# Performance work log

Measured on AMD Instinct MI355X. Metric: run time of the kernel, lower is better.

## Reference

```python
import jax, jax.numpy as jnp
import numpy as np

NUM_STAB = 0.001  # numerical_stabilizer from relu_kernel_transformation


def relu_kernel(data, proj):
    """ReLU random-feature kernel: data [B,L,H,D], proj [M,D] -> [B,L,H,M]."""
    ratio = 1.0 / jnp.sqrt(jnp.asarray(proj.shape[0], jnp.float32))
    data_dash = ratio * jnp.einsum('blhd,md->blhm', data, proj)
    return jax.nn.relu(data_dash) + NUM_STAB


def setup_inputs() -> dict:
    key = jax.random.key(0)
    k1, k2, k3, k4 = jax.random.split(key, 4)
    B, L, H, D, M = 2, 4096, 8, 64, 256
    return {
        'query': jax.random.normal(k1, (B, L, H, D), jnp.float32),
        'key_t': jax.random.normal(k2, (B, L, H, D), jnp.float32),
        'value': jax.random.normal(k3, (B, L, H, D), jnp.float32),
        'projection_matrix': jax.random.normal(k4, (M, D), jnp.float32),
    }


def reference(query, key_t, value, projection_matrix):
    # Kernel feature maps [B,L,H,M]
    qp = relu_kernel(query, projection_matrix)
    kp = relu_kernel(key_t, projection_matrix)
    # Causal path operates in [L,B,H,*] layout
    qs = jnp.transpose(qp, (1, 0, 2, 3))     # [L,B,H,M]
    ks = jnp.transpose(kp, (1, 0, 2, 3))     # [L,B,H,M]
    vs = jnp.transpose(value, (1, 0, 2, 3))  # [L,B,H,D]

    B, H, M = qs.shape[1], qs.shape[2], qs.shape[3]
    D = vs.shape[3]
    init = (jnp.zeros((B, H, M, D), qs.dtype),  # running sum of k outer v
            jnp.zeros((B, H, M), qs.dtype))     # running sum of k

    def step(carry, inp):
        kv_sum, k_sum = carry
        q, k, v = inp  # [B,H,M], [B,H,M], [B,H,D]
        kv_sum = kv_sum + k[..., None] * v[..., None, :]
        k_sum = k_sum + k
        num = jnp.einsum('bhmd,bhm->bhd', kv_sum, q)  # causal numerator step
        den = jnp.einsum('bhm,bhm->bh', q, k_sum)     # causal denominator step
        return (kv_sum, k_sum), (num, den)

    _, (num, den) = jax.lax.scan(step, init, (qs, ks, vs))  # num [L,B,H,D], den [L,B,H]
    den = den[..., None]
    den = jnp.where(den <= 0.0, jnp.ones_like(den), den)
    out = num / den                      # [L,B,H,D]
    return jnp.transpose(out, (1, 0, 2, 3))  # [B,L,H,D]
```

## Files before the change

kernel.cpp:

```cpp
#include <hip/hip_runtime.h>
#include <hip/hip_bf16.h>


#define B_   2
#define L_   4096
#define H_   8
#define D_   64
#define M_   256
#define T_   128
#define C_   (L_ / T_)
#define NBH  (B_ * H_)
#define RATIO 0.0625f
#define STAB  0.001f
#define SVT  136
#define SQS  72

typedef __attribute__((ext_vector_type(8))) short short8;
typedef __attribute__((ext_vector_type(4))) float floatx4;

#define MFMA16(a, b, c) __builtin_amdgcn_mfma_f32_16x16x32_bf16(a, b, c, 0, 0, 0)

__device__ inline unsigned short f2bf(float x) {
    union { float f; unsigned u; } v; v.f = x;
    unsigned r = v.u + 0x7FFF + ((v.u >> 16) & 1);
    return (unsigned short)(r >> 16);
}
__device__ inline unsigned pack2bf(float a, float b) {
    __hip_bfloat162 h = __float22bfloat162_rn(make_float2(a, b));
    unsigned u; __builtin_memcpy(&u, &h, 4);
    return u;
}
__device__ inline short8 ldg8_bfs(const float* p) {
    float4 a = *(const float4*)p;
    float4 b = *(const float4*)(p + 4);
    short8 r;
    r[0] = (short)f2bf(a.x * RATIO); r[1] = (short)f2bf(a.y * RATIO);
    r[2] = (short)f2bf(a.z * RATIO); r[3] = (short)f2bf(a.w * RATIO);
    r[4] = (short)f2bf(b.x * RATIO); r[5] = (short)f2bf(b.y * RATIO);
    r[6] = (short)f2bf(b.z * RATIO); r[7] = (short)f2bf(b.w * RATIO);
    return r;
}
__device__ inline short8 ldg8_bf(const float* p) {
    float4 a = *(const float4*)p;
    float4 b = *(const float4*)(p + 4);
    short8 r;
    r[0] = (short)f2bf(a.x); r[1] = (short)f2bf(a.y);
    r[2] = (short)f2bf(a.z); r[3] = (short)f2bf(a.w);
    r[4] = (short)f2bf(b.x); r[5] = (short)f2bf(b.y);
    r[6] = (short)f2bf(b.z); r[7] = (short)f2bf(b.w);
    return r;
}

__global__ __launch_bounds__(512, 2)
void chunk_kernel(const float* __restrict__ key, const float* __restrict__ val,
                  const float* __restrict__ proj,
                  unsigned short* __restrict__ VTg, unsigned short* __restrict__ Pbf,
                  float* __restrict__ Ppart, float* __restrict__ Zpart) {
    const int c = blockIdx.x, bh = blockIdx.y;
    const int b = bh / H_, h = bh % H_;
    const int tid = threadIdx.x;
    const int w = tid >> 6, lane = tid & 63;
    const int l15 = lane & 15, quad = lane >> 4;

    __shared__ __align__(16) unsigned short VT[64 * SVT];
    __shared__ __align__(16) unsigned short KpT[128 * SVT];
    __shared__ __align__(16) unsigned short KbfL[T_ * D_];

    const size_t rowstr = H_ * D_;
    const size_t base = ((size_t)b * L_ + (size_t)c * T_) * rowstr + (size_t)h * D_;

    for (int i = tid; i < T_ * 8; i += 512) {
        int t = i >> 3, d8 = (i & 7) * 8;
        short8 kv = ldg8_bfs(key + base + (size_t)t * rowstr + d8);
        int rt = t >> 4, l = t & 15, kk = d8 >> 5, q = (d8 & 31) >> 3;
        *(short8*)&KbfL[((rt * 2 + kk) * 64 + q * 16 + l) << 3] = kv;
    }
    for (int i = tid; i < T_ * 16; i += 512) {
        int t = i >> 4, d4 = (i & 15) * 4;
        float4 vv = *(const float4*)(val + base + (size_t)t * rowstr + d4);
        VT[(d4 + 0) * SVT + t] = f2bf(vv.x);
        VT[(d4 + 1) * SVT + t] = f2bf(vv.y);
        VT[(d4 + 2) * SVT + t] = f2bf(vv.z);
        VT[(d4 + 3) * SVT + t] = f2bf(vv.w);
    }
    __syncthreads();
    unsigned short* vout = VTg + ((size_t)bh * C_ + c) * (D_ * T_);
    for (int i = tid; i < D_ * 16; i += 512) {
        int d = i >> 4, t8 = (i & 15) * 8;
        int dt = d >> 4, l = d & 15, k4 = t8 >> 5, q = (t8 & 31) >> 3;
        *(uint4*)(vout + (((dt * 4 + k4) * 64 + q * 16 + l) << 3)) =
            *(const uint4*)&VT[d * SVT + t8];
    }
    if (c == 0 && tid < 256) {
        int i = bh * 256 + tid;
        float4 pv = *(const float4*)(proj + (size_t)i * 4);
        uint2 o; o.x = pack2bf(pv.x, pv.y); o.y = pack2bf(pv.z, pv.w);
        *(uint2*)(Pbf + (size_t)i * 4) = o;
    }

    float* Pp = Ppart + ((size_t)bh * C_ + c) * (D_ * M_);

    for (int half = 0; half < 2; ++half) {
        const int mrow = half * 128 + w * 16 + l15;
        short8 pf0 = ldg8_bf(proj + (size_t)mrow * D_ + quad * 8);
        short8 pf1 = ldg8_bf(proj + (size_t)mrow * D_ + 32 + quad * 8);
        if (half) __syncthreads();
        float zp = 0.f;
#pragma unroll
        for (int rt = 0; rt < 8; ++rt) {
            short8 kf0 = *(const short8*)&KbfL[((rt * 2 + 0) * 64 + lane) << 3];
            short8 kf1 = *(const short8*)&KbfL[((rt * 2 + 1) * 64 + lane) << 3];
            floatx4 a = {0.f, 0.f, 0.f, 0.f};
            a = MFMA16(kf0, pf0, a);
            a = MFMA16(kf1, pf1, a);
            float k0 = fmaxf(a[0], 0.f) + STAB;
            float k1 = fmaxf(a[1], 0.f) + STAB;
            float k2 = fmaxf(a[2], 0.f) + STAB;
            float k3 = fmaxf(a[3], 0.f) + STAB;
            zp += (k0 + k1) + (k2 + k3);
            uint2 pk; pk.x = pack2bf(k0, k1); pk.y = pack2bf(k2, k3);
            *(uint2*)&KpT[(w * 16 + l15) * SVT + rt * 16 + quad * 4] = pk;
        }
        zp += __shfl_xor(zp, 16, 64);
        zp += __shfl_xor(zp, 32, 64);
        if (quad == 0)
            Zpart[((size_t)bh * C_ + c) * M_ + mrow] = zp;
        __syncthreads();

        const int dt_w = w >> 1;
        const int mt0 = (w & 1) * 4;
        short8 vf[4];
#pragma unroll
        for (int k4 = 0; k4 < 4; ++k4)
            vf[k4] = *(const short8*)&VT[(dt_w * 16 + l15) * SVT + k4 * 32 + quad * 8];
#pragma unroll
        for (int mt = 0; mt < 4; ++mt) {
            floatx4 acc = {0.f, 0.f, 0.f, 0.f};
#pragma unroll
            for (int k4 = 0; k4 < 4; ++k4) {
                short8 kb = *(const short8*)&KpT[((mt0 + mt) * 16 + l15) * SVT
                                                 + k4 * 32 + quad * 8];
                acc = MFMA16(vf[k4], kb, acc);
            }
            const int mcol = half * 128 + (mt0 + mt) * 16 + l15;
#pragma unroll
            for (int r = 0; r < 4; ++r)
                Pp[(size_t)(dt_w * 16 + quad * 4 + r) * M_ + mcol] = acc[r];
        }
    }
}

__global__ __launch_bounds__(256, 4)
void prefix_kernel(const float* __restrict__ Ppart, const float* __restrict__ Zpart,
                   unsigned short* __restrict__ S, float* __restrict__ Z) {
    const int g = blockIdx.x, bh = blockIdx.y;
    const int tid = threadIdx.x;
    if (g < 16) {
        const size_t dm = ((size_t)g * 256 + tid) * 4;
        const float* Pp = Ppart + (size_t)bh * C_ * (D_ * M_) + dm;
        unsigned short* Sp = S + (size_t)bh * C_ * (D_ * M_) + dm;
        float4 acc = make_float4(0.f, 0.f, 0.f, 0.f);
#pragma unroll 8
        for (int c = 0; c < C_; ++c) {
            float4 p = *(const float4*)(Pp + (size_t)c * (D_ * M_));
            uint2 o; o.x = pack2bf(acc.x, acc.y); o.y = pack2bf(acc.z, acc.w);
            *(uint2*)(Sp + (size_t)c * (D_ * M_)) = o;
            acc.x += p.x; acc.y += p.y; acc.z += p.z; acc.w += p.w;
        }
    } else {
        const float* Zp = Zpart + (size_t)bh * C_ * M_ + tid;
        float* Zo = Z + (size_t)bh * C_ * M_ + tid;
        float acc = 0.f;
#pragma unroll 8
        for (int c = 0; c < C_; ++c) {
            float z = Zp[(size_t)c * M_];
            Zo[(size_t)c * M_] = acc;
            acc += z;
        }
    }
}

__global__ __launch_bounds__(512, 2)
void phase3_kernel(const float* __restrict__ q, const float* __restrict__ key,
                   const unsigned short* __restrict__ VTg,
                   const unsigned short* __restrict__ Pbf,
                   const unsigned short* __restrict__ S, const float* __restrict__ Z,
                   float* __restrict__ out) {
    const int c = blockIdx.x, bh = blockIdx.y;
    const int b = bh / H_, h = bh % H_;
    const int tid = threadIdx.x;
    const int w = tid >> 6, lane = tid & 63;
    const int l15 = lane & 15, quad = lane >> 4;

    __shared__ __align__(16) unsigned short KpL[T_ * SVT];
    __shared__ __align__(16) unsigned short QpS[8 * 16 * SQS];

    const size_t rowstr = H_ * D_;
    const size_t base = ((size_t)b * L_ + (size_t)c * T_) * rowstr + (size_t)h * D_;
    const unsigned short* Sp = S + (size_t)(bh * C_ + c) * (M_ * D_);
    const float* Zp = Z + (size_t)(bh * C_ + c) * M_;
    const unsigned short* Vc = VTg + ((size_t)bh * C_ + c) * (D_ * T_);

    short8 qf[2], kf[2];
#pragma unroll
    for (int kk = 0; kk < 2; ++kk) {
        size_t ro = base + (size_t)(16 * w + l15) * rowstr + kk * 32 + quad * 8;
        qf[kk] = ldg8_bfs(q + ro);
        kf[kk] = ldg8_bfs(key + ro);
    }

    unsigned short* myQp = QpS + w * 16 * SQS;
    floatx4 num[4];
    floatx4 Aacc[8];
#pragma unroll
    for (int dt = 0; dt < 4; ++dt) { floatx4 z4 = {0.f,0.f,0.f,0.f}; num[dt] = z4; }
#pragma unroll
    for (int ct = 0; ct < 8; ++ct) { floatx4 z4 = {0.f,0.f,0.f,0.f}; Aacc[ct] = z4; }
    float dz[4] = {0.f, 0.f, 0.f, 0.f};

    for (int hh = 0; hh < 2; ++hh) {
        short8 qa[4];
#pragma unroll
        for (int fgl = 0; fgl < 2; ++fgl) {
            const int fg = 2 * hh + fgl;
#pragma unroll
            for (int ct = 0; ct < 4; ++ct) {
                const unsigned short* pp = Pbf + (size_t)(fg * 64 + ct * 16 + l15) * D_;
                short8 pf0 = *(const short8*)(pp + quad * 8);
                short8 pf1 = *(const short8*)(pp + 32 + quad * 8);
                floatx4 aq = {0.f, 0.f, 0.f, 0.f};
                aq = MFMA16(qf[0], pf0, aq);
                aq = MFMA16(qf[1], pf1, aq);
                floatx4 ak = {0.f, 0.f, 0.f, 0.f};
                ak = MFMA16(kf[0], pf0, ak);
                ak = MFMA16(kf[1], pf1, ak);
                const int mloc = fgl * 64 + ct * 16 + l15;
                float zv = Zp[hh * 128 + mloc];
#pragma unroll
                for (int r = 0; r < 4; ++r) {
                    float qpv = fmaxf(aq[r], 0.f) + STAB;
                    float kpv = fmaxf(ak[r], 0.f) + STAB;
                    myQp[(quad * 4 + r) * SQS + ct * 16 + l15] = f2bf(qpv);
                    KpL[(size_t)(16 * w + quad * 4 + r) * SVT + mloc] = f2bf(kpv);
                    dz[r] = fmaf(qpv, zv, dz[r]);
                }
            }
#pragma unroll
            for (int kk = 0; kk < 2; ++kk)
                qa[fgl * 2 + kk] = *(const short8*)&myQp[l15 * SQS + kk * 32 + quad * 8];
        }
#pragma unroll
        for (int dt = 0; dt < 4; ++dt)
#pragma unroll
            for (int kc = 0; kc < 4; ++kc) {
                short8 sb = *(const short8*)(Sp + (size_t)(dt * 16 + l15) * M_
                                             + hh * 128 + kc * 32 + quad * 8);
                num[dt] = MFMA16(qa[kc], sb, num[dt]);
            }
        __syncthreads();
#pragma unroll
        for (int ct = 0; ct < 8; ++ct) {
            if (ct <= w) {
#pragma unroll
                for (int kc = 0; kc < 4; ++kc) {
                    short8 kb = *(const short8*)&KpL[(size_t)(ct * 16 + l15) * SVT
                                                     + kc * 32 + quad * 8];
                    Aacc[ct] = MFMA16(qa[kc], kb, Aacc[ct]);
                }
            }
        }
        __syncthreads();
    }
#pragma unroll
    for (int r = 0; r < 4; ++r) {
        dz[r] += __shfl_xor(dz[r], 1, 64);
        dz[r] += __shfl_xor(dz[r], 2, 64);
        dz[r] += __shfl_xor(dz[r], 4, 64);
        dz[r] += __shfl_xor(dz[r], 8, 64);
    }

    unsigned short* AmL = KpL;
    float da[4] = {0.f, 0.f, 0.f, 0.f};
#pragma unroll
    for (int ct = 0; ct < 8; ++ct)
#pragma unroll
        for (int r = 0; r < 4; ++r) {
            float av = Aacc[ct][r];
            if (ct > w || (ct == w && l15 > quad * 4 + r)) av = 0.f;
            AmL[(size_t)(16 * w + quad * 4 + r) * SVT + ct * 16 + l15] = f2bf(av);
            da[r] += av;
        }
#pragma unroll
    for (int r = 0; r < 4; ++r) {
        da[r] += __shfl_xor(da[r], 1, 64);
        da[r] += __shfl_xor(da[r], 2, 64);
        da[r] += __shfl_xor(da[r], 4, 64);
        da[r] += __shfl_xor(da[r], 8, 64);
    }

    for (int k4 = 0; k4 <= (w >> 1); ++k4) {
        short8 am = *(const short8*)&AmL[(size_t)(16 * w + l15) * SVT
                                         + k4 * 32 + quad * 8];
#pragma unroll
        for (int dt = 0; dt < 4; ++dt) {
            short8 vb = *(const short8*)(Vc + (((size_t)(dt * 4 + k4) * 64 + lane) << 3));
            num[dt] = MFMA16(am, vb, num[dt]);
        }
    }

#pragma unroll
    for (int r = 0; r < 4; ++r) {
        float den = da[r] + dz[r];
        if (den <= 0.f) den = 1.f;
        float inv = 1.f / den;
        int t = 16 * w + quad * 4 + r;
#pragma unroll
        for (int dt = 0; dt < 4; ++dt)
            out[base + (size_t)t * rowstr + dt * 16 + l15] = num[dt][r] * inv;
    }
}

extern "C" void kernel_launch(void* const* d_in, const int* in_sizes, int n_in,
                              void* d_out, int out_size, void* d_ws, size_t ws_size,
                              hipStream_t stream) {
    const float* q    = (const float*)d_in[0];
    const float* k    = (const float*)d_in[1];
    const float* v    = (const float*)d_in[2];
    const float* proj = (const float*)d_in[3];
    float* out = (float*)d_out;

    const size_t nS = (size_t)NBH * C_ * D_ * M_;
    const size_t nZ = (size_t)NBH * C_ * M_;
    const size_t nV = (size_t)NBH * C_ * D_ * T_;
    unsigned short* S     = (unsigned short*)d_ws;
    float*          Z     = (float*)(S + nS);
    unsigned short* VTg   = (unsigned short*)(Z + nZ);
    unsigned short* Pbf   = VTg + nV;
    float*          Ppart = (float*)(Pbf + (size_t)M_ * D_);
    float*          Zpart = Ppart + nS;

    chunk_kernel<<<dim3(C_, NBH), dim3(512), 0, stream>>>(k, v, proj, VTg, Pbf, Ppart, Zpart);
    prefix_kernel<<<dim3(17, NBH), dim3(256), 0, stream>>>(Ppart, Zpart, S, Z);
    phase3_kernel<<<dim3(C_, NBH), dim3(512), 0, stream>>>(q, k, VTg, Pbf, S, Z, out);
}
```

Baseline: 157.0 us.

## Split phase3 over D halves with a z grid dim and relayout VT storage

Phase3 now launches twice as many blocks, each handling half of the D output columns. This raises parallelism from 512 blocks, and launch bounds are raised to 6 blocks per CU. The cost is that each block recomputes the full Q/K feature maps and the intra-chunk attention matrix. The VT buffer is now stored row-major [D][T] instead of the MFMA-fragment-swizzled layout, with phase3 reads adjusted to match. Those reads become strided rather than lane-contiguous.

After: 245.2 us. 1.56x slower.

```diff
diff --git a/kernel.cpp b/kernel.cpp
--- a/kernel.cpp
+++ b/kernel.cpp
@@ -86,10 +86,8 @@
     __syncthreads();
     unsigned short* vout = VTg + ((size_t)bh * C_ + c) * (D_ * T_);
     for (int i = tid; i < D_ * 16; i += 512) {
-        int d = i >> 4, t8 = (i & 15) * 8;
-        int dt = d >> 4, l = d & 15, k4 = t8 >> 5, q = (t8 & 31) >> 3;
-        *(uint4*)(vout + (((dt * 4 + k4) * 64 + q * 16 + l) << 3)) =
-            *(const uint4*)&VT[d * SVT + t8];
+        int d = i >> 4, tt = (i & 15) * 8;
+        *(uint4*)(vout + d * T_ + tt) = *(const uint4*)&VT[d * SVT + tt];
     }
     if (c == 0 && tid < 256) {
         int i = bh * 256 + tid;
@@ -180,13 +178,13 @@
     }
 }
 
-__global__ __launch_bounds__(512, 2)
+__global__ __launch_bounds__(512, 6)
 void phase3_kernel(const float* __restrict__ q, const float* __restrict__ key,
                    const unsigned short* __restrict__ VTg,
                    const unsigned short* __restrict__ Pbf,
                    const unsigned short* __restrict__ S, const float* __restrict__ Z,
                    float* __restrict__ out) {
-    const int c = blockIdx.x, bh = blockIdx.y;
+    const int c = blockIdx.x, bh = blockIdx.y, dh = blockIdx.z;
     const int b = bh / H_, h = bh % H_;
     const int tid = threadIdx.x;
     const int w = tid >> 6, lane = tid & 63;
@@ -210,10 +208,10 @@
     }
 
     unsigned short* myQp = QpS + w * 16 * SQS;
-    floatx4 num[4];
+    floatx4 num[2];
     floatx4 Aacc[8];
 #pragma unroll
-    for (int dt = 0; dt < 4; ++dt) { floatx4 z4 = {0.f,0.f,0.f,0.f}; num[dt] = z4; }
+    for (int dti = 0; dti < 2; ++dti) { floatx4 z4 = {0.f,0.f,0.f,0.f}; num[dti] = z4; }
 #pragma unroll
     for (int ct = 0; ct < 8; ++ct) { floatx4 z4 = {0.f,0.f,0.f,0.f}; Aacc[ct] = z4; }
     float dz[4] = {0.f, 0.f, 0.f, 0.f};
@@ -250,13 +248,15 @@
                 qa[fgl * 2 + kk] = *(const short8*)&myQp[l15 * SQS + kk * 32 + quad * 8];
         }
 #pragma unroll
-        for (int dt = 0; dt < 4; ++dt)
+        for (int dti = 0; dti < 2; ++dti) {
+            const int dt = 2 * dh + dti;
 #pragma unroll
             for (int kc = 0; kc < 4; ++kc) {
                 short8 sb = *(const short8*)(Sp + (size_t)(dt * 16 + l15) * M_
                                              + hh * 128 + kc * 32 + quad * 8);
-                num[dt] = MFMA16(qa[kc], sb, num[dt]);
+                num[dti] = MFMA16(qa[kc], sb, num[dti]);
             }
+        }
         __syncthreads();
 #pragma unroll
         for (int ct = 0; ct < 8; ++ct) {
@@ -302,9 +302,11 @@
         short8 am = *(const short8*)&AmL[(size_t)(16 * w + l15) * SVT
                                          + k4 * 32 + quad * 8];
 #pragma unroll
-        for (int dt = 0; dt < 4; ++dt) {
-            short8 vb = *(const short8*)(Vc + (((size_t)(dt * 4 + k4) * 64 + lane) << 3));
-            num[dt] = MFMA16(am, vb, num[dt]);
+        for (int dti = 0; dti < 2; ++dti) {
+            const int dt = 2 * dh + dti;
+            short8 vb = *(const short8*)(Vc + (size_t)(dt * 16 + l15) * T_
+                                         + k4 * 32 + quad * 8);
+            num[dti] = MFMA16(am, vb, num[dti]);
         }
     }
 
@@ -315,8 +317,8 @@
         float inv = 1.f / den;
         int t = 16 * w + quad * 4 + r;
 #pragma unroll
-        for (int dt = 0; dt < 4; ++dt)
-            out[base + (size_t)t * rowstr + dt * 16 + l15] = num[dt][r] * inv;
+        for (int dti = 0; dti < 2; ++dti)
+            out[base + (size_t)t * rowstr + (2 * dh + dti) * 16 + l15] = num[dti][r] * inv;
     }
 }
 
@@ -341,5 +343,5 @@
 
     chunk_kernel<<<dim3(C_, NBH), dim3(512), 0, stream>>>(k, v, proj, VTg, Pbf, Ppart, Zpart);
     prefix_kernel<<<dim3(17, NBH), dim3(256), 0, stream>>>(Ppart, Zpart, S, Z);
-    phase3_kernel<<<dim3(C_, NBH), dim3(512), 0, stream>>>(q, k, VTg, Pbf, S, Z, out);
-}
+    phase3_kernel<<<dim3(C_, NBH, 2), dim3(512), 0, stream>>>(q, k, VTg, Pbf, S, Z, out);
+}
```
